# Kernel tuning notes

Measured on AMD Instinct MI355X. Metric: run time of the kernel, lower is better.

The kernel has to match this reference:

```python
import jax, jax.numpy as jnp
import numpy as np

D_MODEL = 1024
NUM_HEADS = 16
HEAD_DIM = D_MODEL // NUM_HEADS
B, S = 4, 2048


def setup_inputs() -> dict:
    key = jax.random.key(0)
    ks = jax.random.split(key, 11)
    sc = 1.0 / np.sqrt(D_MODEL)
    return {
        "query": jax.random.normal(ks[0], (B, S, D_MODEL), jnp.float32),
        "key": jax.random.normal(ks[1], (B, S, D_MODEL), jnp.float32),
        "value": jax.random.normal(ks[2], (B, S, D_MODEL), jnp.float32),
        "Wq": jax.random.normal(ks[3], (D_MODEL, D_MODEL), jnp.float32) * sc,
        "bq": jnp.zeros((D_MODEL,), jnp.float32),
        "Wk": jax.random.normal(ks[4], (D_MODEL, D_MODEL), jnp.float32) * sc,
        "bk": jnp.zeros((D_MODEL,), jnp.float32),
        "Wv": jax.random.normal(ks[5], (D_MODEL, D_MODEL), jnp.float32) * sc,
        "bv": jnp.zeros((D_MODEL,), jnp.float32),
        "Wo": jax.random.normal(ks[6], (D_MODEL, D_MODEL), jnp.float32) * sc,
        "bo": jnp.zeros((D_MODEL,), jnp.float32),
    }


def _split_heads(x):
    b, s, _ = x.shape
    return x.reshape(b, s, NUM_HEADS, HEAD_DIM).transpose(0, 2, 1, 3)  # [B,H,S,Dh]


def reference(query, key, value, Wq, bq, Wk, bk, Wv, bv, Wo, bo):
    q = _split_heads(query @ Wq + bq)
    k = _split_heads(key @ Wk + bk)
    v = _split_heads(value @ Wv + bv)
    scores = jnp.einsum("bhqd,bhkd->bhqk", q, k) / np.sqrt(HEAD_DIM)
    attn = jax.nn.softmax(scores, axis=-1)
    out = jnp.einsum("bhqk,bhkd->bhqd", attn, v)
    out = out.transpose(0, 2, 1, 3).reshape(query.shape[0], -1, D_MODEL)
    return out @ Wo + bo
```

## Files before the change

kernel.cpp:

```cpp
#include <hip/hip_runtime.h>

typedef unsigned short u16;
typedef unsigned int   u32;
typedef unsigned long long u64;
typedef __attribute__((ext_vector_type(8))) short bf16x8;
typedef __attribute__((ext_vector_type(4))) float f32x4;

#define S_  2048
#define DH  64
#define DM  1024
#define BS  8192
#define CS  0.18033688011112042f

static __device__ __forceinline__ float bf2f(u16 v){ return __uint_as_float(((u32)v)<<16); }
static __device__ __forceinline__ u16 f2bf(float f){
  u32 x = __float_as_uint(f);
  return (u16)((x + 0x7fffu + ((x>>16)&1u)) >> 16);
}
#if __has_builtin(__builtin_amdgcn_cvt_pk_bf16_f32)
static __device__ __forceinline__ u32 pk2(float x, float y){
  typedef __attribute__((ext_vector_type(2))) __bf16 bf2v;
  union { bf2v v; u32 u; } c; c.v = __builtin_amdgcn_cvt_pk_bf16_f32(x, y); return c.u;
}
#else
static __device__ __forceinline__ u32 pk2(float x, float y){
  return (u32)f2bf(x) | ((u32)f2bf(y) << 16);
}
#endif
#if __has_builtin(__builtin_amdgcn_exp2f)
#define EXP2F(x) __builtin_amdgcn_exp2f(x)
#else
#define EXP2F(x) exp2f(x)
#endif

static __device__ __forceinline__ void dma16(const u16* g, const u16* l){
  __builtin_amdgcn_global_load_lds(
      (const __attribute__((address_space(1))) u32*)(u64)(uintptr_t)g,
      (__attribute__((address_space(3))) u32*)(u32)(u64)(uintptr_t)l, 16, 0, 0);
}

static __device__ __forceinline__ bf16x8 lds_frag(const u16* p){
  union { bf16x8 f; uint2 u[2]; } w;
  w.u[0] = *(const uint2*)(p);
  w.u[1] = *(const uint2*)(p+4);
  return w.f;
}
static __device__ __forceinline__ void stage16_bf(const u16* __restrict__ g, u16* s){
  uint4 a = *(const uint4*)g;
  uint4 b = *(const uint4*)(g+8);
  *(uint2*)(s+0)  = make_uint2(a.x,a.y);
  *(uint2*)(s+4)  = make_uint2(a.z,a.w);
  *(uint2*)(s+8)  = make_uint2(b.x,b.y);
  *(uint2*)(s+12) = make_uint2(b.z,b.w);
}
static __device__ __forceinline__ void stage16_f32(const float* __restrict__ g, u16* s){
  float4 a0 = ((const float4*)g)[0];
  float4 a1 = ((const float4*)g)[1];
  float4 a2 = ((const float4*)g)[2];
  float4 a3 = ((const float4*)g)[3];
  *(uint2*)(s+0)  = make_uint2(pk2(a0.x,a0.y), pk2(a0.z,a0.w));
  *(uint2*)(s+4)  = make_uint2(pk2(a1.x,a1.y), pk2(a1.z,a1.w));
  *(uint2*)(s+8)  = make_uint2(pk2(a2.x,a2.y), pk2(a2.z,a2.w));
  *(uint2*)(s+12) = make_uint2(pk2(a3.x,a3.y), pk2(a3.z,a3.w));
}

__global__ __launch_bounds__(256) void detect_f32(const u16* __restrict__ q, int* flag){
  __shared__ int cnt[256];
  int tid = threadIdx.x;
  int bad = 0;
  for (int i = tid; i < 8192; i += 256){
    u32 e = (q[i] >> 7) & 0xFFu;
    bad += (e == 0xFFu) || (e == 0u);
  }
  cnt[tid] = bad;
  __syncthreads();
  for (int s = 128; s > 0; s >>= 1){ if (tid < s) cnt[tid] += cnt[tid+s]; __syncthreads(); }
  if (tid == 0) flag[0] = (cnt[0] > 0) ? 1 : 0;
}

__global__ __launch_bounds__(256) void transpose4(const void* __restrict__ i0,
    const void* __restrict__ i1, const void* __restrict__ i2, const void* __restrict__ i3,
    u16* o0, u16* o1, u16* o2, u16* o3, const int* __restrict__ flag){
  __shared__ u16 tile[32][33];
  int z = blockIdx.z;
  const void* in = z==0?i0 : z==1?i1 : z==2?i2 : i3;
  u16* out = z==0?o0 : z==1?o1 : z==2?o2 : o3;
  bool f32 = flag[0] != 0;
  int tx = threadIdx.x, ty = threadIdx.y;
  int c  = blockIdx.x*32 + tx;
  int r0 = blockIdx.y*32;
  for (int i=ty;i<32;i+=8){
    long off = (long)(r0+i)*DM + c;
    tile[i][tx] = f32 ? f2bf(((const float*)in)[off]) : ((const u16*)in)[off];
  }
  __syncthreads();
  int rr = r0 + tx, c0 = blockIdx.x*32;
  for (int i=ty;i<32;i+=8) out[(long)(c0+i)*DM + rr] = tile[tx][i];
}

__global__ __launch_bounds__(256) void convert3(const void* __restrict__ a0,
    const void* __restrict__ a1, const void* __restrict__ a2,
    u16* o0, u16* o1, u16* o2, const int* __restrict__ flag){
  int z = blockIdx.z;
  const void* in = z==0?a0 : z==1?a1 : a2;
  u16* out = z==0?o0 : z==1?o1 : o2;
  long i = ((long)blockIdx.x*256 + threadIdx.x)*8;
  if (flag[0]){
    const float4* p = (const float4*)((const float*)in + i);
    float4 x = p[0], y = p[1];
    *(uint4*)(out + i) = make_uint4(pk2(x.x,x.y), pk2(x.z,x.w), pk2(y.x,y.y), pk2(y.z,y.w));
  } else {
    *(uint4*)(out + i) = *(const uint4*)((const u16*)in + i);
  }
}

template<int ADMA>
__global__ __launch_bounds__(256) void gemm_qkv(
    const void* __restrict__ A0, const void* __restrict__ A1, const void* __restrict__ A2,
    const u16* __restrict__ W0, const u16* __restrict__ W1, const u16* __restrict__ W2,
    const void* __restrict__ bv0, const void* __restrict__ bv1, const void* __restrict__ bv2,
    u16* C0, u16* C1, u16* C2, const int* __restrict__ flag){
  constexpr int AST = ADMA ? 32 : 36;
  __shared__ __align__(16) u16 As[128*AST];
  __shared__ __align__(16) u16 Bs[128*32];
  int z = blockIdx.z;
  const void* A  = z==0?A0 : z==1?A1 : A2;
  const u16* BT  = z==0?W0 : z==1?W1 : W2;
  const void* bias = z==0?bv0 : z==1?bv1 : bv2;
  u16* C = z==0?C0 : z==1?C1 : C2;
  const int f = flag[0];
  const bool aF32 = (!ADMA) && (f != 0);
  const bool bF32 = (f != 0);
  int tid = threadIdx.x;
  int by = blockIdx.x, bx = blockIdx.y;
  int lane = tid & 63, w = tid >> 6;
  int t = lane & 15, q = lane >> 4;
  int wr = w >> 1, wc = w & 1;
  f32x4 acc[4][4];
  #pragma unroll
  for(int i=0;i<4;i++) for(int j=0;j<4;j++) for(int k=0;k<4;k++) acc[i][j][k]=0.f;

  const u16* gB = BT + ((long)(bx*128 + w*32 + (lane>>2))*DM + (lane&3)*8);
  const u16* lB = &Bs[(w*32)*32];
  const u16* gA_dma = nullptr; const u16* lA_dma = nullptr;
  long aoff = 0;
  if constexpr (ADMA){
    gA_dma = (const u16*)A + ((long)(by*128 + w*32 + (lane>>2))*DM + (lane&3)*8);
    lA_dma = &As[(w*32)*32];
  } else {
    aoff = (long)(by*128 + (tid>>1))*DM + (tid&1)*16;
  }
  const u16* ArdB = &As[(wr*64 + t)*AST + q*8];
  const u16* BrdB = &Bs[(wc*64 + t)*32  + q*8];

  for (int k0=0; k0<DM; k0+=32){
    dma16(gB + k0, lB);
    dma16(gB + 16*DM + k0, lB + 16*32);
    if constexpr (ADMA){
      dma16(gA_dma + k0, lA_dma);
      dma16(gA_dma + 16*DM + k0, lA_dma + 16*32);
    } else {
      u16* AsW = &As[(tid>>1)*36 + (tid&1)*16];
      if (aF32) stage16_f32((const float*)A + aoff + k0, AsW);
      else      stage16_bf ((const u16*)A  + aoff + k0, AsW);
    }
    __syncthreads();
    bf16x8 af[4], bfr[4];
    #pragma unroll
    for (int rt=0;rt<4;rt++) af[rt]  = lds_frag(ArdB + rt*16*AST);
    #pragma unroll
    for (int ct=0;ct<4;ct++) bfr[ct] = lds_frag(BrdB + ct*16*32);
    #pragma unroll
    for (int rt=0;rt<4;rt++)
      #pragma unroll
      for (int ct=0;ct<4;ct++)
        acc[rt][ct] = __builtin_amdgcn_mfma_f32_16x16x32_bf16(af[rt], bfr[ct], acc[rt][ct], 0,0,0);
    __syncthreads();
  }
  float scale = (z==0) ? CS : 1.0f;
  #pragma unroll
  for (int ct=0;ct<4;ct++){
    int col = bx*128 + wc*64 + ct*16 + t;
    float bvv = bF32 ? ((const float*)bias)[col] : bf2f(((const u16*)bias)[col]);
    #pragma unroll
    for (int rt=0;rt<4;rt++){
      int row0 = by*128 + wr*64 + rt*16 + q*4;
      if (z == 2){
        int bb = row0 >> 11, s = row0 & 2047;
        u32 lo = pk2(acc[rt][ct][0]+bvv, acc[rt][ct][1]+bvv);
        u32 hi = pk2(acc[rt][ct][2]+bvv, acc[rt][ct][3]+bvv);
        *(uint2*)(C + (long)bb*2097152 + (long)col*2048 + s) = make_uint2(lo,hi);
      } else {
        #pragma unroll
        for (int r=0;r<4;r++)
          C[(long)(row0+r)*DM + col] = f2bf((acc[rt][ct][r] + bvv)*scale);
      }
    }
  }
}

__global__ __launch_bounds__(256) void gemm_o(const u16* __restrict__ A,
    const u16* __restrict__ BT, const void* __restrict__ bias, void* __restrict__ C,
    const int* __restrict__ flag){
  __shared__ __align__(16) u16 As[128*32];
  __shared__ __align__(16) u16 Bs[128*32];
  const int f = flag[0];
  int tid = threadIdx.x;
  int by = blockIdx.x, bx = blockIdx.y;
  int lane = tid & 63, w = tid >> 6;
  int t = lane & 15, q = lane >> 4;
  int wr = w >> 1, wc = w & 1;
  f32x4 acc[4][4];
  #pragma unroll
  for(int i=0;i<4;i++) for(int j=0;j<4;j++) for(int k=0;k<4;k++) acc[i][j][k]=0.f;

  const u16* gA = A  + ((long)(by*128 + w*32 + (lane>>2))*DM + (lane&3)*8);
  const u16* gB = BT + ((long)(bx*128 + w*32 + (lane>>2))*DM + (lane&3)*8);
  const u16* lA = &As[(w*32)*32];
  const u16* lB = &Bs[(w*32)*32];
  const u16* ArdB = &As[(wr*64 + t)*32 + q*8];
  const u16* BrdB = &Bs[(wc*64 + t)*32 + q*8];

  for (int k0=0; k0<DM; k0+=32){
    dma16(gA + k0, lA);
    dma16(gA + 16*DM + k0, lA + 16*32);
    dma16(gB + k0, lB);
    dma16(gB + 16*DM + k0, lB + 16*32);
    __syncthreads();
    bf16x8 af[4], bfr[4];
    #pragma unroll
    for (int rt=0;rt<4;rt++) af[rt]  = lds_frag(ArdB + rt*16*32);
    #pragma unroll
    for (int ct=0;ct<4;ct++) bfr[ct] = lds_frag(BrdB + ct*16*32);
    #pragma unroll
    for (int rt=0;rt<4;rt++)
      #pragma unroll
      for (int ct=0;ct<4;ct++)
        acc[rt][ct] = __builtin_amdgcn_mfma_f32_16x16x32_bf16(af[rt], bfr[ct], acc[rt][ct], 0,0,0);
    __syncthreads();
  }
  #pragma unroll
  for (int ct=0;ct<4;ct++){
    int col = bx*128 + wc*64 + ct*16 + t;
    float bvv = f ? ((const float*)bias)[col] : bf2f(((const u16*)bias)[col]);
    #pragma unroll
    for (int rt=0;rt<4;rt++){
      int row0 = by*128 + wr*64 + rt*16 + q*4;
      #pragma unroll
      for (int r=0;r<4;r++){
        long idx = (long)(row0+r)*DM + col;
        float v = acc[rt][ct][r] + bvv;
        if (f) ((float*)C)[idx] = v;
        else   ((u16*)C)[idx]  = f2bf(v);
      }
    }
  }
}

__global__ __launch_bounds__(256) void attn3(const u16* __restrict__ Q,
    const u16* __restrict__ Kb, const u16* __restrict__ Vt, u16* __restrict__ O){
  __shared__ __align__(16) u16 Qs[64*68];
  __shared__ __align__(16) u16 Ks[64*68];
  __shared__ __align__(16) u16 Vs[80*68];
  __shared__ __align__(16) u16 Ps[4][16*68];
  int tid = threadIdx.x;
  int qt = blockIdx.x, bh = blockIdx.y;
  int b = bh >> 4, h = bh & 15;
  int lane = tid & 63, w = tid >> 6;
  int t = lane & 15, q = lane >> 4;
  int sr = tid >> 2, sq = tid & 3;

  stage16_bf(Q + (long)(b*S_ + qt*64 + sr)*DM + h*DH + sq*16, &Qs[sr*68 + sq*16]);
  for (int i = tid; i < 16*68; i += 256){
    int r = i / 68;
    Vs[(64+r)*68 + (i - r*68)] = (r == 0) ? (u16)0x3F80 : (u16)0;
  }

  const u16* Kg = Kb + (long)(b*S_ + sr)*DM + h*DH + sq*16;
  const u16* Vg = Vt + (long)bh*131072 + (long)sr*S_ + sq*16;
  uint4 k0v = *(const uint4*)Kg, k1v = *(const uint4*)(Kg+8);
  uint4 v0v = *(const uint4*)Vg, v1v = *(const uint4*)(Vg+8);

  __syncthreads();
  bf16x8 qf[2];
  qf[0] = lds_frag(&Qs[(w*16+t)*68 + q*8]);
  qf[1] = lds_frag(&Qs[(w*16+t)*68 + 32 + q*8]);

  f32x4 o[4], o4;
  #pragma unroll
  for(int ct=0;ct<4;ct++) for(int r=0;r<4;r++) o[ct][r] = 0.f;
  #pragma unroll
  for(int r=0;r<4;r++) o4[r] = 0.f;
  u16* KsW = &Ks[sr*68 + sq*16];
  u16* VsW = &Vs[sr*68 + sq*16];

  for (int kt=0; kt<32; kt++){
    *(uint2*)(KsW+0)  = make_uint2(k0v.x,k0v.y);
    *(uint2*)(KsW+4)  = make_uint2(k0v.z,k0v.w);
    *(uint2*)(KsW+8)  = make_uint2(k1v.x,k1v.y);
    *(uint2*)(KsW+12) = make_uint2(k1v.z,k1v.w);
    *(uint2*)(VsW+0)  = make_uint2(v0v.x,v0v.y);
    *(uint2*)(VsW+4)  = make_uint2(v0v.z,v0v.w);
    *(uint2*)(VsW+8)  = make_uint2(v1v.x,v1v.y);
    *(uint2*)(VsW+12) = make_uint2(v1v.z,v1v.w);
    __syncthreads();
    if (kt < 31){
      const u16* kg = Kg + (long)(kt+1)*64*DM;
      const u16* vg = Vg + (kt+1)*64;
      k0v = *(const uint4*)kg; k1v = *(const uint4*)(kg+8);
      v0v = *(const uint4*)vg; v1v = *(const uint4*)(vg+8);
    }

    f32x4 sacc[4];
    #pragma unroll
    for(int ct=0;ct<4;ct++) for(int r=0;r<4;r++) sacc[ct][r] = 0.f;
    #pragma unroll
    for (int ct=0;ct<4;ct++){
      #pragma unroll
      for (int ks=0;ks<2;ks++){
        bf16x8 kf = lds_frag(&Ks[(ct*16+t)*68 + ks*32 + q*8]);
        sacc[ct] = __builtin_amdgcn_mfma_f32_16x16x32_bf16(qf[ks], kf, sacc[ct], 0,0,0);
      }
    }
    #pragma unroll
    for (int r=0;r<4;r++){
      float p0 = EXP2F(sacc[0][r]);
      float p1 = EXP2F(sacc[1][r]);
      float p2 = EXP2F(sacc[2][r]);
      float p3 = EXP2F(sacc[3][r]);
      u32 a01 = pk2(p0,p1), a23 = pk2(p2,p3);
      int prow = (q*4+r)*68 + t;
      Ps[w][prow +  0] = (u16)a01;
      Ps[w][prow + 16] = (u16)(a01>>16);
      Ps[w][prow + 32] = (u16)a23;
      Ps[w][prow + 48] = (u16)(a23>>16);
    }
    #pragma unroll
    for (int ks=0;ks<2;ks++){
      bf16x8 pf = lds_frag(&Ps[w][t*68 + ks*32 + q*8]);
      #pragma unroll
      for (int ct=0;ct<4;ct++){
        bf16x8 vf = lds_frag(&Vs[(ct*16+t)*68 + ks*32 + q*8]);
        o[ct] = __builtin_amdgcn_mfma_f32_16x16x32_bf16(pf, vf, o[ct], 0,0,0);
      }
      bf16x8 vf4 = lds_frag(&Vs[(64+t)*68 + ks*32 + q*8]);
      o4 = __builtin_amdgcn_mfma_f32_16x16x32_bf16(pf, vf4, o4, 0,0,0);
    }
    __syncthreads();
  }
  #pragma unroll
  for (int r=0;r<4;r++){
    float l = __shfl(o4[r], lane & 48);
    float inv = 1.f / l;
    int row = qt*64 + w*16 + q*4 + r;
    #pragma unroll
    for (int ct=0;ct<4;ct++)
      O[(long)(b*S_ + row)*DM + h*DH + ct*16 + t] = f2bf(o[ct][r] * inv);
  }
}

extern "C" void kernel_launch(void* const* d_in, const int* in_sizes, int n_in,
                              void* d_out, int out_size, void* d_ws, size_t ws_size,
                              hipStream_t stream){
  (void)in_sizes; (void)n_in; (void)out_size;
  const void* xq = d_in[0];
  const void* xk = d_in[1];
  const void* xv = d_in[2];
  const void* Wq = d_in[3];
  const void* bq = d_in[4];
  const void* Wk = d_in[5];
  const void* bk = d_in[6];
  const void* Wv = d_in[7];
  const void* bv = d_in[8];
  const void* Wo = d_in[9];
  const void* bo = d_in[10];

  int* flag = (int*)d_ws;
  u16* base = (u16*)((char*)d_ws + 256);
  const long NT = (long)BS*DM;
  u16* Qb  = base;
  u16* Kbf = base + NT;
  u16* Vt  = base + 2*NT;
  u16* WqT = base + 3*NT;
  u16* WkT = WqT + (long)DM*DM;
  u16* WvT = WkT + (long)DM*DM;
  u16* WoT = WvT + (long)DM*DM;
  u16* Xc0 = WoT + (long)DM*DM;
  u16* Xc1 = Xc0 + NT;
  u16* Xc2 = Xc1 + NT;
  size_t need_pre = 256 + (size_t)(6*NT + 4*(long)DM*DM)*2;
  bool pre = ws_size >= need_pre;

  detect_f32<<<1, 256, 0, stream>>>((const u16*)xq, flag);

  transpose4<<<dim3(32,32,4), dim3(32,8,1), 0, stream>>>(Wq, Wk, Wv, Wo,
      WqT, WkT, WvT, WoT, flag);

  dim3 gb(256,1,1);
  if (pre){
    convert3<<<dim3(4096,1,3), gb, 0, stream>>>(xq, xk, xv, Xc0, Xc1, Xc2, flag);
    gemm_qkv<1><<<dim3(64,8,3), gb, 0, stream>>>(Xc0, Xc1, Xc2,
        WqT, WkT, WvT, bq, bk, bv, Qb, Kbf, Vt, flag);
  } else {
    gemm_qkv<0><<<dim3(64,8,3), gb, 0, stream>>>(xq, xk, xv,
        WqT, WkT, WvT, bq, bk, bv, Qb, Kbf, Vt, flag);
  }

  attn3<<<dim3(32,64,1), gb, 0, stream>>>(Qb, Kbf, Vt, Qb );

  gemm_o<<<dim3(64,8,1), gb, 0, stream>>>(Qb, WoT, bo, d_out, flag);
}
```

Baseline: 421.6 us.

## Rewrite attention with double-buffered LDS DMA, swizzled layout, and 128-row query tiles

Replaces the attention kernel with a version that loads K and V tiles straight into LDS through global_load_lds into a double buffer, so the next tile's load overlaps the current tile's compute. Shared-memory tiles use an XOR swizzle and 128-bit fragment reads, and the V-transpose output from the QKV GEMM is written pre-permuted to match that swizzle. Each wave now handles 32 query rows, which halves the grid and reuses each K/V fragment for two row tiles. The row sum is accumulated from the exponentials and reduced with shuffles, replacing the ones-column MFMA trick. The costs are more register pressure, scalar 2-byte scattered stores for V, and the absence of max subtraction, which the previous kernel also lacked.

```diff
diff --git a/kernel.cpp b/kernel.cpp
--- a/kernel.cpp
+++ b/kernel.cpp
@@ -43,6 +43,11 @@
   union { bf16x8 f; uint2 u[2]; } w;
   w.u[0] = *(const uint2*)(p);
   w.u[1] = *(const uint2*)(p+4);
+  return w.f;
+}
+static __device__ __forceinline__ bf16x8 frag16v(const u16* p){
+  union { bf16x8 f; uint4 u; } w;
+  w.u = *(const uint4*)p;
   return w.f;
 }
 static __device__ __forceinline__ void stage16_bf(const u16* __restrict__ g, u16* s){
@@ -187,9 +192,11 @@
       int row0 = by*128 + wr*64 + rt*16 + q*4;
       if (z == 2){
         int bb = row0 >> 11, s = row0 & 2047;
-        u32 lo = pk2(acc[rt][ct][0]+bvv, acc[rt][ct][1]+bvv);
-        u32 hi = pk2(acc[rt][ct][2]+bvv, acc[rt][ct][3]+bvv);
-        *(uint2*)(C + (long)bb*2097152 + (long)col*2048 + s) = make_uint2(lo,hi);
+        long vbase = (long)bb*2097152 + (long)col*2048
+                   + (s & ~63) + ((s & 15) << 2) + ((s >> 4) & 3);
+        #pragma unroll
+        for (int r=0;r<4;r++)
+          C[vbase + r*4] = f2bf(acc[rt][ct][r] + bvv);
       } else {
         #pragma unroll
         for (int r=0;r<4;r++)
@@ -257,105 +264,130 @@
   }
 }
 
-__global__ __launch_bounds__(256) void attn3(const u16* __restrict__ Q,
+__global__ __launch_bounds__(256,3) void attn4(const u16* __restrict__ Q,
     const u16* __restrict__ Kb, const u16* __restrict__ Vt, u16* __restrict__ O){
-  __shared__ __align__(16) u16 Qs[64*68];
-  __shared__ __align__(16) u16 Ks[64*68];
-  __shared__ __align__(16) u16 Vs[80*68];
-  __shared__ __align__(16) u16 Ps[4][16*68];
+  __shared__ __align__(16) u16 Ks[2][4096];
+  __shared__ __align__(16) u16 Vs[2][4096];
+  __shared__ __align__(16) u16 Ps[4][2304];
   int tid = threadIdx.x;
   int qt = blockIdx.x, bh = blockIdx.y;
   int b = bh >> 4, h = bh & 15;
   int lane = tid & 63, w = tid >> 6;
   int t = lane & 15, q = lane >> 4;
-  int sr = tid >> 2, sq = tid & 3;
-
-  stage16_bf(Q + (long)(b*S_ + qt*64 + sr)*DM + h*DH + sq*16, &Qs[sr*68 + sq*16]);
-  for (int i = tid; i < 16*68; i += 256){
-    int r = i / 68;
-    Vs[(64+r)*68 + (i - r*68)] = (r == 0) ? (u16)0x3F80 : (u16)0;
-  }
-
-  const u16* Kg = Kb + (long)(b*S_ + sr)*DM + h*DH + sq*16;
-  const u16* Vg = Vt + (long)bh*131072 + (long)sr*S_ + sq*16;
-  uint4 k0v = *(const uint4*)Kg, k1v = *(const uint4*)(Kg+8);
-  uint4 v0v = *(const uint4*)Vg, v1v = *(const uint4*)(Vg+8);
-
-  __syncthreads();
-  bf16x8 qf[2];
-  qf[0] = lds_frag(&Qs[(w*16+t)*68 + q*8]);
-  qf[1] = lds_frag(&Qs[(w*16+t)*68 + 32 + q*8]);
-
-  f32x4 o[4], o4;
-  #pragma unroll
-  for(int ct=0;ct<4;ct++) for(int r=0;r<4;r++) o[ct][r] = 0.f;
-  #pragma unroll
-  for(int r=0;r<4;r++) o4[r] = 0.f;
-  u16* KsW = &Ks[sr*68 + sq*16];
-  u16* VsW = &Vs[sr*68 + sq*16];
+
+  const u16* Qbase = Q + ((long)(b*S_ + qt*128 + w*32 + t)*DM + h*DH + q*8);
+  bf16x8 qf[2][2];
+  qf[0][0] = frag16v(Qbase);
+  qf[0][1] = frag16v(Qbase + 32);
+  qf[1][0] = frag16v(Qbase + 16*DM);
+  qf[1][1] = frag16v(Qbase + 16*DM + 32);
+
+  int r0 = tid >> 3;
+  int cb = ((tid & 7) * 16) ^ ((r0 & 7) << 4);
+  const char* gK = (const char*)Kb + (((long)(b*S_ + r0)*DM + h*DH) << 1) + cb;
+  const char* gV = (const char*)Vt + ((((long)bh << 17) + ((long)r0 << 11)) << 1) + cb;
+  const long gK1 = ((long)32*DM) << 1;
+  const long gV1 = ((long)32*S_) << 1;
+  const int ld0 = w*512, ld1 = 2048 + w*512;
+
+  f32x4 o[2][4];
+  #pragma unroll
+  for (int i=0;i<2;i++) for (int j=0;j<4;j++) for (int k=0;k<4;k++) o[i][j][k]=0.f;
+  f32x4 lsum[2];
+  #pragma unroll
+  for (int i=0;i<2;i++) for (int k=0;k<4;k++) lsum[i][k]=0.f;
+
+  const int xorv = (t & 7) << 4;
+
+  dma16((const u16*)(gK),       &Ks[0][ld0]);
+  dma16((const u16*)(gK + gK1), &Ks[0][ld1]);
+  dma16((const u16*)(gV),       &Vs[0][ld0]);
+  dma16((const u16*)(gV + gV1), &Vs[0][ld1]);
 
   for (int kt=0; kt<32; kt++){
-    *(uint2*)(KsW+0)  = make_uint2(k0v.x,k0v.y);
-    *(uint2*)(KsW+4)  = make_uint2(k0v.z,k0v.w);
-    *(uint2*)(KsW+8)  = make_uint2(k1v.x,k1v.y);
-    *(uint2*)(KsW+12) = make_uint2(k1v.z,k1v.w);
-    *(uint2*)(VsW+0)  = make_uint2(v0v.x,v0v.y);
-    *(uint2*)(VsW+4)  = make_uint2(v0v.z,v0v.w);
-    *(uint2*)(VsW+8)  = make_uint2(v1v.x,v1v.y);
-    *(uint2*)(VsW+12) = make_uint2(v1v.z,v1v.w);
-    __syncthreads();
+    int cur = kt & 1;
     if (kt < 31){
-      const u16* kg = Kg + (long)(kt+1)*64*DM;
-      const u16* vg = Vg + (kt+1)*64;
-      k0v = *(const uint4*)kg; k1v = *(const uint4*)(kg+8);
-      v0v = *(const uint4*)vg; v1v = *(const uint4*)(vg+8);
-    }
-
-    f32x4 sacc[4];
-    #pragma unroll
-    for(int ct=0;ct<4;ct++) for(int r=0;r<4;r++) sacc[ct][r] = 0.f;
-    #pragma unroll
-    for (int ct=0;ct<4;ct++){
-      #pragma unroll
-      for (int ks=0;ks<2;ks++){
-        bf16x8 kf = lds_frag(&Ks[(ct*16+t)*68 + ks*32 + q*8]);
-        sacc[ct] = __builtin_amdgcn_mfma_f32_16x16x32_bf16(qf[ks], kf, sacc[ct], 0,0,0);
+      long ko = ((long)(kt+1)*64*DM) << 1;
+      long vo = (long)(kt+1) << 7;
+      dma16((const u16*)(gK + ko),       &Ks[cur^1][ld0]);
+      dma16((const u16*)(gK + ko + gK1), &Ks[cur^1][ld1]);
+      dma16((const u16*)(gV + vo),       &Vs[cur^1][ld0]);
+      dma16((const u16*)(gV + vo + gV1), &Vs[cur^1][ld1]);
+      asm volatile("s_waitcnt vmcnt(4)" ::: "memory");
+    } else {
+      asm volatile("s_waitcnt vmcnt(0)" ::: "memory");
+    }
+    __builtin_amdgcn_s_barrier();
+
+    const u16* Kc = Ks[cur];
+    const u16* Vc = Vs[cur];
+
+    f32x4 sacc[2][4];
+    #pragma unroll
+    for (int i=0;i<2;i++) for (int j=0;j<4;j++) for (int k=0;k<4;k++) sacc[i][j][k]=0.f;
+    #pragma unroll
+    for (int ks=0; ks<2; ks++){
+      int off = ((ks*64 + q*16) ^ xorv) >> 1;
+      bf16x8 k0 = frag16v(Kc + (t     )*64 + off);
+      bf16x8 k1 = frag16v(Kc + (16 + t)*64 + off);
+      bf16x8 k2 = frag16v(Kc + (32 + t)*64 + off);
+      bf16x8 k3 = frag16v(Kc + (48 + t)*64 + off);
+      #pragma unroll
+      for (int rt=0; rt<2; rt++){
+        sacc[rt][0] = __builtin_amdgcn_mfma_f32_16x16x32_bf16(qf[rt][ks], k0, sacc[rt][0],0,0,0);
+        sacc[rt][1] = __builtin_amdgcn_mfma_f32_16x16x32_bf16(qf[rt][ks], k1, sacc[rt][1],0,0,0);
+        sacc[rt][2] = __builtin_amdgcn_mfma_f32_16x16x32_bf16(qf[rt][ks], k2, sacc[rt][2],0,0,0);
+        sacc[rt][3] = __builtin_amdgcn_mfma_f32_16x16x32_bf16(qf[rt][ks], k3, sacc[rt][3],0,0,0);
       }
     }
-    #pragma unroll
-    for (int r=0;r<4;r++){
-      float p0 = EXP2F(sacc[0][r]);
-      float p1 = EXP2F(sacc[1][r]);
-      float p2 = EXP2F(sacc[2][r]);
-      float p3 = EXP2F(sacc[3][r]);
-      u32 a01 = pk2(p0,p1), a23 = pk2(p2,p3);
-      int prow = (q*4+r)*68 + t;
-      Ps[w][prow +  0] = (u16)a01;
-      Ps[w][prow + 16] = (u16)(a01>>16);
-      Ps[w][prow + 32] = (u16)a23;
-      Ps[w][prow + 48] = (u16)(a23>>16);
-    }
-    #pragma unroll
-    for (int ks=0;ks<2;ks++){
-      bf16x8 pf = lds_frag(&Ps[w][t*68 + ks*32 + q*8]);
-      #pragma unroll
-      for (int ct=0;ct<4;ct++){
-        bf16x8 vf = lds_frag(&Vs[(ct*16+t)*68 + ks*32 + q*8]);
-        o[ct] = __builtin_amdgcn_mfma_f32_16x16x32_bf16(pf, vf, o[ct], 0,0,0);
+
+    #pragma unroll
+    for (int rt=0; rt<2; rt++){
+      #pragma unroll
+      for (int r=0; r<4; r++){
+        float p0 = EXP2F(sacc[rt][0][r]);
+        float p1 = EXP2F(sacc[rt][1][r]);
+        float p2 = EXP2F(sacc[rt][2][r]);
+        float p3 = EXP2F(sacc[rt][3][r]);
+        lsum[rt][r] += (p0+p1)+(p2+p3);
+        *(uint2*)&Ps[w][(rt*16 + q*4 + r)*72 + t*4] = make_uint2(pk2(p0,p1), pk2(p2,p3));
       }
-      bf16x8 vf4 = lds_frag(&Vs[(64+t)*68 + ks*32 + q*8]);
-      o4 = __builtin_amdgcn_mfma_f32_16x16x32_bf16(pf, vf4, o4, 0,0,0);
-    }
-    __syncthreads();
-  }
-  #pragma unroll
-  for (int r=0;r<4;r++){
-    float l = __shfl(o4[r], lane & 48);
-    float inv = 1.f / l;
-    int row = qt*64 + w*16 + q*4 + r;
-    #pragma unroll
-    for (int ct=0;ct<4;ct++)
-      O[(long)(b*S_ + row)*DM + h*DH + ct*16 + t] = f2bf(o[ct][r] * inv);
+    }
+
+    #pragma unroll
+    for (int ks=0; ks<2; ks++){
+      int off = ((ks*64 + q*16) ^ xorv) >> 1;
+      bf16x8 v0 = frag16v(Vc + (t     )*64 + off);
+      bf16x8 v1 = frag16v(Vc + (16 + t)*64 + off);
+      bf16x8 v2 = frag16v(Vc + (32 + t)*64 + off);
+      bf16x8 v3 = frag16v(Vc + (48 + t)*64 + off);
+      #pragma unroll
+      for (int rt=0; rt<2; rt++){
+        bf16x8 pf = frag16v(&Ps[w][(rt*16 + t)*72 + ks*32 + q*8]);
+        o[rt][0] = __builtin_amdgcn_mfma_f32_16x16x32_bf16(pf, v0, o[rt][0],0,0,0);
+        o[rt][1] = __builtin_amdgcn_mfma_f32_16x16x32_bf16(pf, v1, o[rt][1],0,0,0);
+        o[rt][2] = __builtin_amdgcn_mfma_f32_16x16x32_bf16(pf, v2, o[rt][2],0,0,0);
+        o[rt][3] = __builtin_amdgcn_mfma_f32_16x16x32_bf16(pf, v3, o[rt][3],0,0,0);
+      }
+    }
+    __builtin_amdgcn_s_barrier();
+  }
+
+  #pragma unroll
+  for (int rt=0; rt<2; rt++){
+    #pragma unroll
+    for (int r=0; r<4; r++){
+      float l = lsum[rt][r];
+      l += __shfl_xor(l, 1);
+      l += __shfl_xor(l, 2);
+      l += __shfl_xor(l, 4);
+      l += __shfl_xor(l, 8);
+      float inv = 1.f / l;
+      int row = qt*128 + w*32 + rt*16 + q*4 + r;
+      #pragma unroll
+      for (int ct=0; ct<4; ct++)
+        O[(long)(b*S_ + row)*DM + h*DH + ct*16 + t] = f2bf(o[rt][ct][r] * inv);
+    }
   }
 }
 
@@ -406,7 +438,7 @@
         WqT, WkT, WvT, bq, bk, bv, Qb, Kbf, Vt, flag);
   }
 
-  attn3<<<dim3(32,64,1), gb, 0, stream>>>(Qb, Kbf, Vt, Qb );
+  attn4<<<dim3(16,64,1), gb, 0, stream>>>(Qb, Kbf, Vt, Qb );
 
   gemm_o<<<dim3(64,8,1), gb, 0, stream>>>(Qb, WoT, bo, d_out, flag);
 }
```

Result: faster. 388.7 us (-7.8%).
